# Kernel optimization log

Hardware: AMD Instinct MI355X
Metric: run time of the kernel (lower is better)

The kernel has to match this reference:

```python
import jax, jax.numpy as jnp
import numpy as np

EMBED_DIM = 768
HEADS = 8
HEAD_DIM = 128  # gnn_hidden_dim
OUT_DIM = HEADS * HEAD_DIM  # 1024, concat=True
NEG_SLOPE = 0.2  # PyG GATConv leaky_relu slope


def setup_inputs() -> dict:
    key = jax.random.key(0)
    ks = jax.random.split(key, 12)
    N, E = 10000, 160000
    x = jax.random.normal(ks[0], (N, EMBED_DIM), dtype=jnp.float32)
    edge_index = jax.random.randint(ks[1], (2, E), 0, N, dtype=jnp.int32)
    edge_attr = jax.random.uniform(ks[2], (E, 1), dtype=jnp.float32)
    # GATConv params (single layer, edge_dim=1)
    sc = 1.0 / np.sqrt(EMBED_DIM)
    W = jax.random.normal(ks[3], (EMBED_DIM, OUT_DIM), dtype=jnp.float32) * sc
    att_src = jax.random.normal(ks[4], (HEADS, HEAD_DIM), dtype=jnp.float32) * 0.1
    att_dst = jax.random.normal(ks[5], (HEADS, HEAD_DIM), dtype=jnp.float32) * 0.1
    W_edge = jax.random.normal(ks[6], (1, OUT_DIM), dtype=jnp.float32)
    att_edge = jax.random.normal(ks[7], (HEADS, HEAD_DIM), dtype=jnp.float32) * 0.1
    bias = jnp.zeros((OUT_DIM,), dtype=jnp.float32)
    # final classifier: in = 3*OUT_DIM (global pool + text node + image node)
    clf_W = jax.random.normal(ks[8], (3 * OUT_DIM, 2), dtype=jnp.float32) * (1.0 / np.sqrt(3 * OUT_DIM))
    clf_b = jnp.zeros((2,), dtype=jnp.float32)
    return {
        'x': x, 'edge_index': edge_index, 'edge_attr': edge_attr,
        'text_idx': 0, 'image_idx': 1,
        'W': W, 'att_src': att_src, 'att_dst': att_dst,
        'W_edge': W_edge, 'att_edge': att_edge, 'bias': bias,
        'clf_W': clf_W, 'clf_b': clf_b,
    }


def gat_layer(x, edge_index, edge_attr, W, att_src, att_dst, W_edge, att_edge, bias):
    N = x.shape[0]
    # add self-loops with edge_attr = mean of existing edge_attr (PyG default fill_value='mean')
    loop = jnp.arange(N, dtype=edge_index.dtype)
    ei = jnp.concatenate([edge_index, jnp.stack([loop, loop])], axis=1)
    ea_mean = jnp.mean(edge_attr, axis=0, keepdims=True)
    ea = jnp.concatenate([edge_attr, jnp.broadcast_to(ea_mean, (N, edge_attr.shape[1]))], axis=0)
    src, dst = ei[0], ei[1]
    xs = (x @ W).reshape(N, HEADS, HEAD_DIM)             # [N, H, C]
    a_src = jnp.einsum('nhc,hc->nh', xs, att_src)        # per-node src logits
    a_dst = jnp.einsum('nhc,hc->nh', xs, att_dst)
    e_emb = (ea @ W_edge).reshape(-1, HEADS, HEAD_DIM)   # [Etot, H, C]
    a_edge = jnp.einsum('ehc,hc->eh', e_emb, att_edge)
    alpha = jax.nn.leaky_relu(a_src[src] + a_dst[dst] + a_edge, NEG_SLOPE)  # [Etot, H]
    # softmax over incoming edges of each dst node
    m = jax.ops.segment_max(alpha, dst, num_segments=N)
    ex = jnp.exp(alpha - m[dst])
    denom = jax.ops.segment_sum(ex, dst, num_segments=N)
    w = ex / denom[dst]                                  # normalized attention [Etot, H]
    msg = xs[src] * w[:, :, None]                        # [Etot, H, C]
    out = jax.ops.segment_sum(msg, dst, num_segments=N)  # [N, H, C]
    return out.reshape(N, OUT_DIM) + bias


def reference(x, edge_index, edge_attr, text_idx, image_idx,
              W, att_src, att_dst, W_edge, att_edge, bias, clf_W, clf_b):
    # single GAT layer (num_gat_layers=1 -> no ELU/dropout after, eval mode)
    h = gat_layer(x, edge_index, edge_attr, W, att_src, att_dst, W_edge, att_edge, bias)
    g = jnp.mean(h, axis=0, keepdims=True)               # global_mean_pool, batch=None
    t = h[text_idx][None, :]
    im = h[image_idx][None, :]
    fused = jnp.concatenate([g, t, im], axis=1)          # [1, 3*OUT_DIM]
    logits = fused @ clf_W + clf_b                       # [1, 2]
    return logits
```

## Files before the change

kernel.cpp:

```cpp
#include <hip/hip_runtime.h>

#define NN 10000
#define EE 160000
#define ETOT (EE + NN)
#define EMB 768
#define ODIM 1024
#define NEG 0.2f
#define CAP 56

#define OFF_P      0
#define OFF_Q      12288
#define OFF_EAACC  12296
#define OFF_CNTD   12304
#define OFF_CNTS   22304
#define ZERO_START 12296
#define ZERO_CNT   20008
#define OFF_A      32304
#define OFF_APART  192304
#define OFF_SRCD   1472304
#define OFF_DSTS   2032304
#define OFF_PACK   2592304
#define OFF_EXD    2762304
#define OFF_EXS    7242304
#define OFF_RDEN   11722304
#define OFF_S      11802304
#define OFF_Z      11882304
#define OFF_YPART  11894592
#define OFF_FPART  12859200

__global__ __launch_bounds__(256) void k1f(
    const float* __restrict__ W, const float* __restrict__ att_src,
    const float* __restrict__ att_dst, const float* __restrict__ W_edge,
    const float* __restrict__ att_edge, const float* __restrict__ edge_attr,
    const int* __restrict__ ei, float* __restrict__ ws) {
  int b = blockIdx.x;
  if (b < 48) {
    int tid = b * 256 + threadIdx.x;
    int k = tid >> 4, j = tid & 15, h = j & 7;
    const float* att = (j < 8) ? att_src : att_dst;
    const float* wp = W + k * ODIM + h * 128;
    const float* ap = att + h * 128;
    float acc = 0.f;
    #pragma unroll 8
    for (int c = 0; c < 128; ++c) acc += wp[c] * ap[c];
    ws[OFF_P + k * 16 + j] = acc;
  } else if (b == 48) {
    if (threadIdx.x < 8) {
      int h = threadIdx.x;
      float acc = 0.f;
      #pragma unroll 8
      for (int c = 0; c < 128; ++c) acc += W_edge[h * 128 + c] * att_edge[h * 128 + c];
      ws[OFF_Q + h] = acc;
    }
  } else if (b < 113) {
    int bi = b - 49;
    float acc = 0.f;
    for (int i = bi * 256 + threadIdx.x; i < EE; i += 64 * 256) acc += edge_attr[i];
    #pragma unroll
    for (int off = 32; off > 0; off >>= 1) acc += __shfl_down(acc, off, 64);
    if ((threadIdx.x & 63) == 0) atomicAdd(&ws[OFF_EAACC], acc);
  } else {
    int e = (b - 113) * 256 + threadIdx.x;
    if (e >= ETOT) return;
    int src, dst;
    if (e < EE) { src = ei[e]; dst = ei[EE + e]; } else { src = dst = e - EE; }
    int* cntd = (int*)(ws + OFF_CNTD);
    int* cnts = (int*)(ws + OFF_CNTS);
    int pd = atomicAdd(&cntd[dst], 1);
    if (pd < CAP) ((int*)(ws + OFF_SRCD))[dst * CAP + pd] = src;
    int ps = atomicAdd(&cnts[src], 1);
    if (ps < CAP) ((int*)(ws + OFF_DSTS))[src * CAP + ps] = dst;
    ((int*)(ws + OFF_PACK))[e] = (pd & 0xffff) | (ps << 16);
  }
}

__global__ __launch_bounds__(256) void k3_part(const float* __restrict__ x,
                                               float* __restrict__ ws) {
  __shared__ float pL[96 * 16];
  const int c = blockIdx.y;
  const int kbase = c * 96;
  for (int i = threadIdx.x; i < 96 * 16; i += 256) pL[i] = ws[OFF_P + kbase * 16 + i];
  __syncthreads();
  int n = blockIdx.x * 256 + threadIdx.x;
  if (n >= NN) return;
  float acc[16];
  #pragma unroll
  for (int j = 0; j < 16; ++j) acc[j] = 0.f;
  const float4* xr = (const float4*)(x + n * EMB + kbase);
  for (int kk = 0; kk < 24; ++kk) {
    float4 xv = xr[kk];
    const float* pr = &pL[kk * 64];
    #pragma unroll
    for (int j = 0; j < 16; ++j) acc[j] += xv.x * pr[j];
    #pragma unroll
    for (int j = 0; j < 16; ++j) acc[j] += xv.y * pr[16 + j];
    #pragma unroll
    for (int j = 0; j < 16; ++j) acc[j] += xv.z * pr[32 + j];
    #pragma unroll
    for (int j = 0; j < 16; ++j) acc[j] += xv.w * pr[48 + j];
  }
  float4* ap = (float4*)(ws + OFF_APART + c * 160000 + n * 16);
  ap[0] = make_float4(acc[0], acc[1], acc[2], acc[3]);
  ap[1] = make_float4(acc[4], acc[5], acc[6], acc[7]);
  ap[2] = make_float4(acc[8], acc[9], acc[10], acc[11]);
  ap[3] = make_float4(acc[12], acc[13], acc[14], acc[15]);
}

__global__ __launch_bounds__(256) void k_reduceA(float* __restrict__ ws) {
  int i = blockIdx.x * 256 + threadIdx.x;
  if (i >= 40000) return;
  float4 r = make_float4(0.f, 0.f, 0.f, 0.f);
  #pragma unroll
  for (int c = 0; c < 8; ++c) {
    float4 a = ((const float4*)(ws + OFF_APART + c * 160000))[i];
    r.x += a.x; r.y += a.y; r.z += a.z; r.w += a.w;
  }
  ((float4*)(ws + OFF_A))[i] = r;
}

__global__ __launch_bounds__(256) void kE(const int* __restrict__ ei,
                                          const float* __restrict__ edge_attr,
                                          float* __restrict__ ws) {
  int e = blockIdx.x * 256 + threadIdx.x;
  if (e >= ETOT) return;
  int src, dst; float ea;
  if (e < EE) { src = ei[e]; dst = ei[EE + e]; ea = edge_attr[e]; }
  else { src = dst = e - EE; ea = ws[OFF_EAACC] * (1.0f / EE); }
  int pk = ((const int*)(ws + OFF_PACK))[e];
  int pd = pk & 0xffff, ps = pk >> 16;
  const float4* as4 = (const float4*)(ws + OFF_A + src * 16);
  const float4* ad4 = (const float4*)(ws + OFF_A + dst * 16 + 8);
  float4 s0 = as4[0], s1 = as4[1], d0 = ad4[0], d1 = ad4[1];
  float asrc[8] = {s0.x, s0.y, s0.z, s0.w, s1.x, s1.y, s1.z, s1.w};
  float adst[8] = {d0.x, d0.y, d0.z, d0.w, d1.x, d1.y, d1.z, d1.w};
  float ex[8];
  #pragma unroll
  for (int h = 0; h < 8; ++h) {
    float v = asrc[h] + adst[h] + ea * ws[OFF_Q + h];
    v = (v >= 0.f) ? v : NEG * v;
    ex[h] = __expf(v);
  }
  float4 e0 = make_float4(ex[0], ex[1], ex[2], ex[3]);
  float4 e1 = make_float4(ex[4], ex[5], ex[6], ex[7]);
  if (pd < CAP) {
    float4* p = (float4*)(ws + OFF_EXD + (dst * CAP + pd) * 8);
    p[0] = e0; p[1] = e1;
  }
  if (ps < CAP) {
    float4* p = (float4*)(ws + OFF_EXS + (src * CAP + ps) * 8);
    p[0] = e0; p[1] = e1;
  }
}

__global__ __launch_bounds__(256) void kD(float* __restrict__ ws) {
  int t = blockIdx.x * 256 + threadIdx.x;
  if (t >= NN * 8) return;
  int dst = t >> 3, h = t & 7;
  int deg = ((const int*)(ws + OFF_CNTD))[dst];
  if (deg > CAP) deg = CAP;
  const float* base = ws + OFF_EXD + dst * (CAP * 8) + h;
  float den = 0.f;
  for (int j = 0; j < deg; ++j) den += base[j * 8];
  ws[OFF_RDEN + dst * 8 + h] = 1.0f / den;
}

__global__ __launch_bounds__(256) void kSZ(const float* __restrict__ x,
                                           const int* __restrict__ tptr,
                                           const int* __restrict__ iptr,
                                           float* __restrict__ ws) {
  if (blockIdx.x < 313) {
    int t = blockIdx.x * 256 + threadIdx.x;
    if (t >= NN * 8) return;
    int src = t >> 3, h = t & 7;
    int deg = ((const int*)(ws + OFF_CNTS))[src];
    if (deg > CAP) deg = CAP;
    const int* dstrow = (const int*)(ws + OFF_DSTS) + src * CAP;
    const float* exrow = ws + OFF_EXS + src * (CAP * 8) + h;
    float s = 0.f;
    for (int j = 0; j < deg; ++j)
      s += exrow[j * 8] * ws[OFF_RDEN + dstrow[j] * 8 + h];
    ws[OFF_S + src * 8 + h] = s;
  } else {
    __shared__ float wL[CAP * 8];
    __shared__ int srcS[CAP];
    __shared__ int degS;
    int r = blockIdx.x - 313;
    int d = r / 3, ky = r % 3;
    int target = (d == 0) ? tptr[0] : iptr[0];
    if (threadIdx.x == 0) {
      int dg = ((const int*)(ws + OFF_CNTD))[target];
      degS = (dg > CAP) ? CAP : dg;
    }
    __syncthreads();
    int deg = degS;
    for (int idx = threadIdx.x; idx < deg * 8; idx += 256) {
      int j = idx >> 3, h = idx & 7;
      wL[idx] = ws[OFF_EXD + (target * CAP + j) * 8 + h]
              * ws[OFF_RDEN + target * 8 + h];
      if (h == 0) srcS[j] = ((const int*)(ws + OFF_SRCD))[target * CAP + j];
    }
    __syncthreads();
    int col = ky * 256 + threadIdx.x;
    float acc[8];
    #pragma unroll
    for (int h = 0; h < 8; ++h) acc[h] = 0.f;
    for (int j = 0; j < deg; ++j) {
      float xv = x[srcS[j] * EMB + col];
      const float* wv = &wL[j * 8];
      #pragma unroll
      for (int h = 0; h < 8; ++h) acc[h] += wv[h] * xv;
    }
    #pragma unroll
    for (int h = 0; h < 8; ++h) ws[OFF_Z + (d * 8 + h) * EMB + col] = acc[h];
  }
}

__global__ __launch_bounds__(256) void k7s(const float* __restrict__ x,
                                           float* __restrict__ ws) {
  __shared__ float sL[64 * 8];
  int base = blockIdx.x * 64;
  int c = blockIdx.y;
  for (int i = threadIdx.x; i < 512; i += 256) {
    int n = base + (i >> 3);
    sL[i] = (n < NN) ? ws[OFF_S + base * 8 + i] : 0.f;
  }
  __syncthreads();
  int col = c * 256 + threadIdx.x;
  float acc[8];
  #pragma unroll
  for (int h = 0; h < 8; ++h) acc[h] = 0.f;
  int nmax = (NN - base < 64) ? (NN - base) : 64;
  for (int i = 0; i < nmax; ++i) {
    float xv = x[(base + i) * EMB + col];
    const float* sv = &sL[i * 8];
    #pragma unroll
    for (int h = 0; h < 8; ++h) acc[h] += xv * sv[h];
  }
  float* yp = ws + OFF_YPART + (blockIdx.x * 3 + c) * 2048;
  #pragma unroll
  for (int h = 0; h < 8; ++h) yp[h * 256 + threadIdx.x] = acc[h];
}

__global__ __launch_bounds__(128) void k8_part(const float* __restrict__ W,
                                               float* __restrict__ ws) {
  __shared__ float vL[3 * 96];
  int h = blockIdx.x, kc = blockIdx.y;
  int kbase = kc * 96;
  for (int k = threadIdx.x; k < 96; k += 128) {
    int col = kbase + k, cc = col >> 8, ck = col & 255;
    float acc = 0.f;
    for (int b = 0; b < 157; ++b)
      acc += ws[OFF_YPART + (b * 3 + cc) * 2048 + h * 256 + ck];
    vL[k] = acc * (1.0f / NN);
  }
  for (int i = threadIdx.x; i < 192; i += 128) {
    int d = i / 96, k = i - d * 96;
    vL[96 + i] = ws[OFF_Z + (d * 8 + h) * EMB + kbase + k];
  }
  __syncthreads();
  int c = threadIdx.x;
  float a0 = 0.f, a1 = 0.f, a2 = 0.f;
  #pragma unroll 4
  for (int k = 0; k < 96; ++k) {
    float wv = W[(kbase + k) * ODIM + h * 128 + c];
    a0 += vL[k] * wv;
    a1 += vL[96 + k] * wv;
    a2 += vL[192 + k] * wv;
  }
  float* fp = ws + OFF_FPART + kc * 3072 + h * 128 + c;
  fp[0] = a0; fp[1024] = a1; fp[2048] = a2;
}

__global__ __launch_bounds__(256) void k9_logits(const float* __restrict__ clf_W,
                                                 const float* __restrict__ clf_b,
                                                 const float* __restrict__ bias,
                                                 const float* __restrict__ ws,
                                                 float* __restrict__ out) {
  float a0 = 0.f, a1 = 0.f;
  for (int i = threadIdx.x; i < 3072; i += 256) {
    float f = bias[i & 1023];
    #pragma unroll
    for (int kc = 0; kc < 8; ++kc) f += ws[OFF_FPART + kc * 3072 + i];
    a0 += f * clf_W[i * 2 + 0];
    a1 += f * clf_W[i * 2 + 1];
  }
  #pragma unroll
  for (int off = 32; off > 0; off >>= 1) {
    a0 += __shfl_down(a0, off, 64);
    a1 += __shfl_down(a1, off, 64);
  }
  __shared__ float r0[4], r1[4];
  int wid = threadIdx.x >> 6, lane = threadIdx.x & 63;
  if (lane == 0) { r0[wid] = a0; r1[wid] = a1; }
  __syncthreads();
  if (threadIdx.x == 0) {
    out[0] = r0[0] + r0[1] + r0[2] + r0[3] + clf_b[0];
    out[1] = r1[0] + r1[1] + r1[2] + r1[3] + clf_b[1];
  }
}

extern "C" void kernel_launch(void* const* d_in, const int* in_sizes, int n_in,
                              void* d_out, int out_size, void* d_ws, size_t ws_size,
                              hipStream_t stream) {
  const float* x        = (const float*)d_in[0];
  const int*   ei       = (const int*)d_in[1];
  const float* edge_attr= (const float*)d_in[2];
  const int*   tptr     = (const int*)d_in[3];
  const int*   iptr     = (const int*)d_in[4];
  const float* W        = (const float*)d_in[5];
  const float* att_src  = (const float*)d_in[6];
  const float* att_dst  = (const float*)d_in[7];
  const float* W_edge   = (const float*)d_in[8];
  const float* att_edge = (const float*)d_in[9];
  const float* bias     = (const float*)d_in[10];
  const float* clf_W    = (const float*)d_in[11];
  const float* clf_b    = (const float*)d_in[12];
  float* ws  = (float*)d_ws;
  float* out = (float*)d_out;

  hipMemsetAsync(ws + ZERO_START, 0, ZERO_CNT * sizeof(float), stream);
  k1f<<<778, 256, 0, stream>>>(W, att_src, att_dst, W_edge, att_edge, edge_attr, ei, ws);
  dim3 g3(40, 8);
  k3_part<<<g3, 256, 0, stream>>>(x, ws);
  k_reduceA<<<157, 256, 0, stream>>>(ws);
  kE<<<665, 256, 0, stream>>>(ei, edge_attr, ws);
  kD<<<313, 256, 0, stream>>>(ws);
  kSZ<<<319, 256, 0, stream>>>(x, tptr, iptr, ws);
  dim3 g7(157, 3);
  k7s<<<g7, 256, 0, stream>>>(x, ws);
  dim3 g8(8, 8);
  k8_part<<<g8, 128, 0, stream>>>(W, ws);
  k9_logits<<<1, 256, 0, stream>>>(clf_W, clf_b, bias, ws, out);
}
```

Baseline: 200.2 us.

## Fuse node-logit GEMV with in-block reduction and merge classifier into final kernel

Replaces the split-K node-logit kernel and its separate reduce pass with one kernel that computes all K chunks per block and reduces them through shared memory. The bias-only logit term is computed in an extra block of the edge kernel, and the final projection kernel now applies the classifier directly and atomically adds into the output. This removes two launches and the partial-sum buffers. Block sizes are halved for the edge, denominator and S kernels. Correctness now depends on the output being initialised by the extra block in kE before k8's atomics run.

```diff
diff --git a/kernel.cpp b/kernel.cpp
--- a/kernel.cpp
+++ b/kernel.cpp
@@ -16,17 +16,15 @@
 #define ZERO_START 12296
 #define ZERO_CNT   20008
 #define OFF_A      32304
-#define OFF_APART  192304
-#define OFF_SRCD   1472304
-#define OFF_DSTS   2032304
-#define OFF_PACK   2592304
-#define OFF_EXD    2762304
-#define OFF_EXS    7242304
-#define OFF_RDEN   11722304
-#define OFF_S      11802304
-#define OFF_Z      11882304
-#define OFF_YPART  11894592
-#define OFF_FPART  12859200
+#define OFF_SRCD   192304
+#define OFF_DSTS   752304
+#define OFF_PACK   1312304
+#define OFF_EXD    1482304
+#define OFF_EXS    5962304
+#define OFF_RDEN   10442304
+#define OFF_S      10522304
+#define OFF_Z      10602304
+#define OFF_YPART  10614592
 
 __global__ __launch_bounds__(256) void k1f(
     const float* __restrict__ W, const float* __restrict__ att_src,
@@ -70,107 +68,133 @@
     if (pd < CAP) ((int*)(ws + OFF_SRCD))[dst * CAP + pd] = src;
     int ps = atomicAdd(&cnts[src], 1);
     if (ps < CAP) ((int*)(ws + OFF_DSTS))[src * CAP + ps] = dst;
-    ((int*)(ws + OFF_PACK))[e] = (pd & 0xffff) | (ps << 16);
-  }
-}
-
-__global__ __launch_bounds__(256) void k3_part(const float* __restrict__ x,
-                                               float* __restrict__ ws) {
-  __shared__ float pL[96 * 16];
-  const int c = blockIdx.y;
-  const int kbase = c * 96;
-  for (int i = threadIdx.x; i < 96 * 16; i += 256) pL[i] = ws[OFF_P + kbase * 16 + i];
-  __syncthreads();
-  int n = blockIdx.x * 256 + threadIdx.x;
-  if (n >= NN) return;
-  float acc[16];
-  #pragma unroll
-  for (int j = 0; j < 16; ++j) acc[j] = 0.f;
-  const float4* xr = (const float4*)(x + n * EMB + kbase);
-  for (int kk = 0; kk < 24; ++kk) {
-    float4 xv = xr[kk];
-    const float* pr = &pL[kk * 64];
-    #pragma unroll
-    for (int j = 0; j < 16; ++j) acc[j] += xv.x * pr[j];
-    #pragma unroll
-    for (int j = 0; j < 16; ++j) acc[j] += xv.y * pr[16 + j];
-    #pragma unroll
-    for (int j = 0; j < 16; ++j) acc[j] += xv.z * pr[32 + j];
-    #pragma unroll
-    for (int j = 0; j < 16; ++j) acc[j] += xv.w * pr[48 + j];
-  }
-  float4* ap = (float4*)(ws + OFF_APART + c * 160000 + n * 16);
-  ap[0] = make_float4(acc[0], acc[1], acc[2], acc[3]);
-  ap[1] = make_float4(acc[4], acc[5], acc[6], acc[7]);
-  ap[2] = make_float4(acc[8], acc[9], acc[10], acc[11]);
-  ap[3] = make_float4(acc[12], acc[13], acc[14], acc[15]);
-}
-
-__global__ __launch_bounds__(256) void k_reduceA(float* __restrict__ ws) {
-  int i = blockIdx.x * 256 + threadIdx.x;
-  if (i >= 40000) return;
-  float4 r = make_float4(0.f, 0.f, 0.f, 0.f);
-  #pragma unroll
-  for (int c = 0; c < 8; ++c) {
-    float4 a = ((const float4*)(ws + OFF_APART + c * 160000))[i];
-    r.x += a.x; r.y += a.y; r.z += a.z; r.w += a.w;
-  }
-  ((float4*)(ws + OFF_A))[i] = r;
-}
-
-__global__ __launch_bounds__(256) void kE(const int* __restrict__ ei,
+    if (pd > CAP) pd = CAP;
+    if (ps > CAP) ps = CAP;
+    ((int*)(ws + OFF_PACK))[e] = pd | (ps << 16);
+  }
+}
+
+__global__ __launch_bounds__(256) void kAx(const float* __restrict__ x,
+                                           float* __restrict__ ws) {
+  __shared__ float smem[12288];
+  for (int i = threadIdx.x; i < 3072; i += 256)
+    ((float4*)smem)[i] = ((const float4*)(ws + OFF_P))[i];
+  __syncthreads();
+  int nl = threadIdx.x & 31, cg = threadIdx.x >> 5;
+  int n = blockIdx.x * 32 + nl;
+  float a[16];
+  #pragma unroll
+  for (int j = 0; j < 16; ++j) a[j] = 0.f;
+  if (n < NN) {
+    const float4* xr = (const float4*)(x + n * EMB + cg * 96);
+    for (int kk = 0; kk < 24; ++kk) {
+      float4 xv = xr[kk];
+      const float* pr = &smem[(cg * 96 + kk * 4) * 16];
+      #pragma unroll
+      for (int j = 0; j < 16; ++j) a[j] += xv.x * pr[j];
+      #pragma unroll
+      for (int j = 0; j < 16; ++j) a[j] += xv.y * pr[16 + j];
+      #pragma unroll
+      for (int j = 0; j < 16; ++j) a[j] += xv.z * pr[32 + j];
+      #pragma unroll
+      for (int j = 0; j < 16; ++j) a[j] += xv.w * pr[48 + j];
+    }
+  }
+  __syncthreads();
+  #pragma unroll
+  for (int j = 0; j < 16; ++j) smem[(cg * 16 + j) * 33 + nl] = a[j];
+  __syncthreads();
+  for (int w = threadIdx.x; w < 512; w += 256) {
+    int rnl = w >> 4, j = w & 15;
+    int nn = blockIdx.x * 32 + rnl;
+    if (nn < NN) {
+      float s = 0.f;
+      #pragma unroll
+      for (int c2 = 0; c2 < 8; ++c2) s += smem[(c2 * 16 + j) * 33 + rnl];
+      ws[OFF_A + nn * 16 + j] = s;
+    }
+  }
+}
+
+__global__ __launch_bounds__(128) void kE(const int* __restrict__ ei,
                                           const float* __restrict__ edge_attr,
+                                          const float* __restrict__ bias,
+                                          const float* __restrict__ clf_W,
+                                          const float* __restrict__ clf_b,
+                                          float* __restrict__ out,
                                           float* __restrict__ ws) {
-  int e = blockIdx.x * 256 + threadIdx.x;
-  if (e >= ETOT) return;
-  int src, dst; float ea;
-  if (e < EE) { src = ei[e]; dst = ei[EE + e]; ea = edge_attr[e]; }
-  else { src = dst = e - EE; ea = ws[OFF_EAACC] * (1.0f / EE); }
-  int pk = ((const int*)(ws + OFF_PACK))[e];
-  int pd = pk & 0xffff, ps = pk >> 16;
-  const float4* as4 = (const float4*)(ws + OFF_A + src * 16);
-  const float4* ad4 = (const float4*)(ws + OFF_A + dst * 16 + 8);
-  float4 s0 = as4[0], s1 = as4[1], d0 = ad4[0], d1 = ad4[1];
-  float asrc[8] = {s0.x, s0.y, s0.z, s0.w, s1.x, s1.y, s1.z, s1.w};
-  float adst[8] = {d0.x, d0.y, d0.z, d0.w, d1.x, d1.y, d1.z, d1.w};
-  float ex[8];
-  #pragma unroll
-  for (int h = 0; h < 8; ++h) {
-    float v = asrc[h] + adst[h] + ea * ws[OFF_Q + h];
-    v = (v >= 0.f) ? v : NEG * v;
-    ex[h] = __expf(v);
-  }
-  float4 e0 = make_float4(ex[0], ex[1], ex[2], ex[3]);
-  float4 e1 = make_float4(ex[4], ex[5], ex[6], ex[7]);
-  if (pd < CAP) {
-    float4* p = (float4*)(ws + OFF_EXD + (dst * CAP + pd) * 8);
-    p[0] = e0; p[1] = e1;
-  }
-  if (ps < CAP) {
-    float4* p = (float4*)(ws + OFF_EXS + (src * CAP + ps) * 8);
-    p[0] = e0; p[1] = e1;
-  }
-}
-
-__global__ __launch_bounds__(256) void kD(float* __restrict__ ws) {
-  int t = blockIdx.x * 256 + threadIdx.x;
-  if (t >= NN * 8) return;
+  __shared__ float red[4];
+  int* wsI = (int*)ws;
+  if (blockIdx.x < 1329) {
+    int e = blockIdx.x * 128 + threadIdx.x;
+    if (e >= ETOT) return;
+    int src, dst; float ea;
+    if (e < EE) { src = ei[e]; dst = ei[EE + e]; ea = edge_attr[e]; }
+    else { src = dst = e - EE; ea = ws[OFF_EAACC] * (1.0f / EE); }
+    int pk = wsI[OFF_PACK + e];
+    int pd = pk & 0xffff, ps = pk >> 16;
+    const float4* as4 = (const float4*)(ws + OFF_A + src * 16);
+    const float4* ad4 = (const float4*)(ws + OFF_A + dst * 16 + 8);
+    float4 s0 = as4[0], s1 = as4[1], d0 = ad4[0], d1 = ad4[1];
+    float asr[8] = {s0.x, s0.y, s0.z, s0.w, s1.x, s1.y, s1.z, s1.w};
+    float ads[8] = {d0.x, d0.y, d0.z, d0.w, d1.x, d1.y, d1.z, d1.w};
+    float ex[8];
+    #pragma unroll
+    for (int h = 0; h < 8; ++h) {
+      float v = asr[h] + ads[h] + ea * ws[OFF_Q + h];
+      v = (v >= 0.f) ? v : NEG * v;
+      ex[h] = __expf(v);
+    }
+    float4 e0 = make_float4(ex[0], ex[1], ex[2], ex[3]);
+    float4 e1 = make_float4(ex[4], ex[5], ex[6], ex[7]);
+    if (pd < CAP) {
+      float4* p = (float4*)(ws + OFF_EXD + (dst * CAP + pd) * 8);
+      p[0] = e0; p[1] = e1;
+    }
+    if (ps < CAP) {
+      float4* p = (float4*)(ws + OFF_EXS + (src * CAP + ps) * 8);
+      p[0] = e0; p[1] = e1;
+    }
+  } else {
+    int t = threadIdx.x;
+    float b0 = 0.f, b1 = 0.f;
+    for (int i = t; i < 3072; i += 128) {
+      float f = bias[i & 1023];
+      b0 += f * clf_W[2 * i];
+      b1 += f * clf_W[2 * i + 1];
+    }
+    #pragma unroll
+    for (int o = 32; o > 0; o >>= 1) {
+      b0 += __shfl_down(b0, o, 64);
+      b1 += __shfl_down(b1, o, 64);
+    }
+    if ((t & 63) == 0) { red[(t >> 6) * 2] = b0; red[(t >> 6) * 2 + 1] = b1; }
+    __syncthreads();
+    if (t == 0) {
+      out[0] = clf_b[0] + red[0] + red[2];
+      out[1] = clf_b[1] + red[1] + red[3];
+    }
+  }
+}
+
+__global__ __launch_bounds__(128) void kD(float* __restrict__ ws) {
+  int t = blockIdx.x * 128 + threadIdx.x;
   int dst = t >> 3, h = t & 7;
   int deg = ((const int*)(ws + OFF_CNTD))[dst];
   if (deg > CAP) deg = CAP;
   const float* base = ws + OFF_EXD + dst * (CAP * 8) + h;
   float den = 0.f;
   for (int j = 0; j < deg; ++j) den += base[j * 8];
-  ws[OFF_RDEN + dst * 8 + h] = 1.0f / den;
-}
-
-__global__ __launch_bounds__(256) void kSZ(const float* __restrict__ x,
+  ws[OFF_RDEN + t] = 1.0f / den;
+}
+
+__global__ __launch_bounds__(128) void kSZ(const float* __restrict__ x,
                                            const int* __restrict__ tptr,
                                            const int* __restrict__ iptr,
                                            float* __restrict__ ws) {
-  if (blockIdx.x < 313) {
-    int t = blockIdx.x * 256 + threadIdx.x;
-    if (t >= NN * 8) return;
+  __shared__ float sm[512];
+  if (blockIdx.x < 625) {
+    int t = blockIdx.x * 128 + threadIdx.x;
     int src = t >> 3, h = t & 7;
     int deg = ((const int*)(ws + OFF_CNTS))[src];
     if (deg > CAP) deg = CAP;
@@ -179,28 +203,28 @@
     float s = 0.f;
     for (int j = 0; j < deg; ++j)
       s += exrow[j * 8] * ws[OFF_RDEN + dstrow[j] * 8 + h];
-    ws[OFF_S + src * 8 + h] = s;
+    ws[OFF_S + t] = s;
   } else {
-    __shared__ float wL[CAP * 8];
-    __shared__ int srcS[CAP];
-    __shared__ int degS;
-    int r = blockIdx.x - 313;
-    int d = r / 3, ky = r % 3;
+    float* wL = sm;
+    int* srcS = (int*)(sm + 448);
+    int* degP = (int*)(sm + 508);
+    int r = blockIdx.x - 625;
+    int d = r / 6, kc = r % 6;
     int target = (d == 0) ? tptr[0] : iptr[0];
     if (threadIdx.x == 0) {
       int dg = ((const int*)(ws + OFF_CNTD))[target];
-      degS = (dg > CAP) ? CAP : dg;
+      degP[0] = (dg > CAP) ? CAP : dg;
     }
     __syncthreads();
-    int deg = degS;
-    for (int idx = threadIdx.x; idx < deg * 8; idx += 256) {
+    int deg = degP[0];
+    for (int idx = threadIdx.x; idx < deg * 8; idx += 128) {
       int j = idx >> 3, h = idx & 7;
       wL[idx] = ws[OFF_EXD + (target * CAP + j) * 8 + h]
               * ws[OFF_RDEN + target * 8 + h];
       if (h == 0) srcS[j] = ((const int*)(ws + OFF_SRCD))[target * CAP + j];
     }
     __syncthreads();
-    int col = ky * 256 + threadIdx.x;
+    int col = kc * 128 + threadIdx.x;
     float acc[8];
     #pragma unroll
     for (int h = 0; h < 8; ++h) acc[h] = 0.f;
@@ -236,66 +260,59 @@
     #pragma unroll
     for (int h = 0; h < 8; ++h) acc[h] += xv * sv[h];
   }
-  float* yp = ws + OFF_YPART + (blockIdx.x * 3 + c) * 2048;
-  #pragma unroll
-  for (int h = 0; h < 8; ++h) yp[h * 256 + threadIdx.x] = acc[h];
-}
-
-__global__ __launch_bounds__(128) void k8_part(const float* __restrict__ W,
-                                               float* __restrict__ ws) {
-  __shared__ float vL[3 * 96];
-  int h = blockIdx.x, kc = blockIdx.y;
-  int kbase = kc * 96;
-  for (int k = threadIdx.x; k < 96; k += 128) {
-    int col = kbase + k, cc = col >> 8, ck = col & 255;
-    float acc = 0.f;
-    for (int b = 0; b < 157; ++b)
-      acc += ws[OFF_YPART + (b * 3 + cc) * 2048 + h * 256 + ck];
-    vL[k] = acc * (1.0f / NN);
-  }
-  for (int i = threadIdx.x; i < 192; i += 128) {
-    int d = i / 96, k = i - d * 96;
-    vL[96 + i] = ws[OFF_Z + (d * 8 + h) * EMB + kbase + k];
+  float* yp = ws + OFF_YPART + blockIdx.x * 6144 + col;
+  #pragma unroll
+  for (int h = 0; h < 8; ++h) yp[h * 768] = acc[h];
+}
+
+__global__ __launch_bounds__(128) void k8(const float* __restrict__ W,
+                                          const float* __restrict__ clf_W,
+                                          float* __restrict__ out,
+                                          float* __restrict__ ws) {
+  __shared__ float vL[144];
+  __shared__ float red[4];
+  int h = blockIdx.x, kc = blockIdx.y, kbase = kc * 48;
+  for (int i = threadIdx.x; i < 144; i += 128) {
+    int d = i / 48, k = i - d * 48;
+    float v;
+    if (d == 0) {
+      float acc = 0.f;
+      for (int b = 0; b < 157; ++b)
+        acc += ws[OFF_YPART + b * 6144 + h * 768 + kbase + k];
+      v = acc * (1.0f / NN);
+    } else {
+      v = ws[OFF_Z + ((d - 1) * 8 + h) * 768 + kbase + k];
+    }
+    vL[i] = v;
   }
   __syncthreads();
   int c = threadIdx.x;
   float a0 = 0.f, a1 = 0.f, a2 = 0.f;
   #pragma unroll 4
-  for (int k = 0; k < 96; ++k) {
+  for (int k = 0; k < 48; ++k) {
     float wv = W[(kbase + k) * ODIM + h * 128 + c];
     a0 += vL[k] * wv;
-    a1 += vL[96 + k] * wv;
-    a2 += vL[192 + k] * wv;
-  }
-  float* fp = ws + OFF_FPART + kc * 3072 + h * 128 + c;
-  fp[0] = a0; fp[1024] = a1; fp[2048] = a2;
-}
-
-__global__ __launch_bounds__(256) void k9_logits(const float* __restrict__ clf_W,
-                                                 const float* __restrict__ clf_b,
-                                                 const float* __restrict__ bias,
-                                                 const float* __restrict__ ws,
-                                                 float* __restrict__ out) {
-  float a0 = 0.f, a1 = 0.f;
-  for (int i = threadIdx.x; i < 3072; i += 256) {
-    float f = bias[i & 1023];
-    #pragma unroll
-    for (int kc = 0; kc < 8; ++kc) f += ws[OFF_FPART + kc * 3072 + i];
-    a0 += f * clf_W[i * 2 + 0];
-    a1 += f * clf_W[i * 2 + 1];
-  }
-  #pragma unroll
-  for (int off = 32; off > 0; off >>= 1) {
-    a0 += __shfl_down(a0, off, 64);
-    a1 += __shfl_down(a1, off, 64);
-  }
-  __shared__ float r0[4], r1[4];
-  int wid = threadIdx.x >> 6, lane = threadIdx.x & 63;
-  if (lane == 0) { r0[wid] = a0; r1[wid] = a1; }
+    a1 += vL[48 + k] * wv;
+    a2 += vL[96 + k] * wv;
+  }
+  int ib = h * 128 + c;
+  float l0 = a0 * clf_W[2 * ib] + a1 * clf_W[2 * (1024 + ib)]
+           + a2 * clf_W[2 * (2048 + ib)];
+  float l1 = a0 * clf_W[2 * ib + 1] + a1 * clf_W[2 * (1024 + ib) + 1]
+           + a2 * clf_W[2 * (2048 + ib) + 1];
+  #pragma unroll
+  for (int o = 32; o > 0; o >>= 1) {
+    l0 += __shfl_down(l0, o, 64);
+    l1 += __shfl_down(l1, o, 64);
+  }
+  if ((threadIdx.x & 63) == 0) {
+    red[(threadIdx.x >> 6) * 2] = l0;
+    red[(threadIdx.x >> 6) * 2 + 1] = l1;
+  }
   __syncthreads();
   if (threadIdx.x == 0) {
-    out[0] = r0[0] + r0[1] + r0[2] + r0[3] + clf_b[0];
-    out[1] = r1[0] + r1[1] + r1[2] + r1[3] + clf_b[1];
+    atomicAdd(&out[0], red[0] + red[2]);
+    atomicAdd(&out[1], red[1] + red[3]);
   }
 }
 
@@ -320,15 +337,12 @@
 
   hipMemsetAsync(ws + ZERO_START, 0, ZERO_CNT * sizeof(float), stream);
   k1f<<<778, 256, 0, stream>>>(W, att_src, att_dst, W_edge, att_edge, edge_attr, ei, ws);
-  dim3 g3(40, 8);
-  k3_part<<<g3, 256, 0, stream>>>(x, ws);
-  k_reduceA<<<157, 256, 0, stream>>>(ws);
-  kE<<<665, 256, 0, stream>>>(ei, edge_attr, ws);
-  kD<<<313, 256, 0, stream>>>(ws);
-  kSZ<<<319, 256, 0, stream>>>(x, tptr, iptr, ws);
+  kAx<<<313, 256, 0, stream>>>(x, ws);
+  kE<<<1330, 128, 0, stream>>>(ei, edge_attr, bias, clf_W, clf_b, out, ws);
+  kD<<<625, 128, 0, stream>>>(ws);
+  kSZ<<<637, 128, 0, stream>>>(x, tptr, iptr, ws);
   dim3 g7(157, 3);
   k7s<<<g7, 256, 0, stream>>>(x, ws);
-  dim3 g8(8, 8);
-  k8_part<<<g8, 128, 0, stream>>>(W, ws);
-  k9_logits<<<1, 256, 0, stream>>>(clf_W, clf_b, bias, ws, out);
-}
+  dim3 g8(8, 16);
+  k8<<<g8, 128, 0, stream>>>(W, clf_W, out, ws);
+}
```

Result: faster. 192.7 us (-3.7%).
